# Optimization experiments

Measured on AMD Instinct MI355X. Metric: run time of the kernel, lower is better.

Reference implementation:

```python
import jax, jax.numpy as jnp
import numpy as np

NUM_EMBEDDINGS = 8192
EMBEDDING_DIM = 64
COMMITMENT_COST = 0.25


def setup_inputs() -> dict:
    key = jax.random.key(0)
    kx, ke = jax.random.split(key)
    x = jax.random.normal(kx, (32, 1024, EMBEDDING_DIM), dtype=jnp.float32)
    embeddings = jax.random.normal(ke, (NUM_EMBEDDINGS, EMBEDDING_DIM), dtype=jnp.float32)
    return {"x": x, "embeddings": embeddings}


def reference(x, embeddings):
    d = embeddings.shape[1]
    flat_x = x.reshape(-1, d)  # [N, D]
    # squared euclidean distances (argmin identical to cdist argmin):
    d2 = (
        jnp.sum(flat_x * flat_x, axis=-1, keepdims=True)
        - 2.0 * flat_x @ embeddings.T
        + jnp.sum(embeddings * embeddings, axis=-1)
    )
    encoding_indices = jnp.argmin(d2, axis=1)  # [N]
    quantized = embeddings[encoding_indices].reshape(x.shape)
    codebook_loss = jnp.mean((jax.lax.stop_gradient(quantized) - x) ** 2)
    commitment_loss = COMMITMENT_COST * jnp.mean((quantized - jax.lax.stop_gradient(x)) ** 2)
    loss = codebook_loss + commitment_loss
    # straight-through estimator
    quantized_st = x + jax.lax.stop_gradient(quantized - x)
    return quantized_st, loss, encoding_indices
```

## Files before the change

### kernel.cpp

```cpp
#include <hip/hip_runtime.h>
#include <hip/hip_bf16.h>
#include <float.h>

#define N_ROWS 32768
#define DIMS   64
#define K_EMB  8192
#define NT     (K_EMB / 16)
#define NQ     4
#define NTQ    (NT / NQ)
#define TSTAGE 4
#define NSTAGE (NTQ / TSTAGE)
#define GAP_THR 1.5e-3f

typedef __attribute__((ext_vector_type(8))) short s8v;
typedef __attribute__((ext_vector_type(4))) float f4v;
typedef __attribute__((ext_vector_type(4))) int   i4v;

#define WS_EFRAG 0
#define WS_EN2   (2 * 1024 * 1024)
#define WS_IDX   (WS_EN2 + K_EMB * 4)
#define WS_KEY   (WS_IDX + N_ROWS * 4)
#define WS_BH    (WS_KEY + N_ROWS * 8)
#define WS_SH    (WS_BH + 4 * N_ROWS * 4)
#define WS_CH    (WS_SH + 4 * N_ROWS * 4)
#define WS_CTL   (WS_CH + 4 * N_ROWS * 4)
#define WS_WL    (WS_CTL + 16)

#define OUT_LOSS (N_ROWS * DIMS)
#define OUT_IDX  (N_ROWS * DIMS + 1)

__device__ inline short bfh(float v) {
    __hip_bfloat16 h = __float2bfloat16(v);
    return __builtin_bit_cast(short, h);
}
__device__ inline float bff(short s) {
    __hip_bfloat16 h = __builtin_bit_cast(__hip_bfloat16, s);
    return __bfloat162float(h);
}

__global__ void vq_prep(const float* __restrict__ emb, short* __restrict__ efrag,
                        float* __restrict__ en2) {
    int gid = blockIdx.x * 256 + threadIdx.x;
    int t = gid >> 6, lane = gid & 63;
    int m = lane & 15, q = lane >> 4;
    const float* er = emb + (size_t)(t * 16 + m) * DIMS;
    s8v hi0, lo0, hi1, lo1;
    float ss = 0.f;
#pragma unroll
    for (int j = 0; j < 8; ++j) {
        float v0 = er[q * 8 + j];
        float v1 = er[32 + q * 8 + j];
        ss += v0 * v0 + v1 * v1;
        short h0 = bfh(v0); lo0[j] = bfh(v0 - bff(h0)); hi0[j] = h0;
        short h1 = bfh(v1); lo1[j] = bfh(v1 - bff(h1)); hi1[j] = h1;
    }
    s8v* base = (s8v*)efrag + (size_t)t * 4 * 64;
    base[0 * 64 + lane] = hi0;
    base[1 * 64 + lane] = hi1;
    base[2 * 64 + lane] = lo0;
    base[3 * 64 + lane] = lo1;
    ss += __shfl_xor(ss, 16, 64);
    ss += __shfl_xor(ss, 32, 64);
    if (q == 0) en2[t * 16 + m] = -0.5f * ss;
}

__global__ __launch_bounds__(256, 4) void vq_phase1(
    const float* __restrict__ x, const short* __restrict__ efrag,
    const float* __restrict__ en2,
    float* __restrict__ bh, float* __restrict__ sh, int* __restrict__ ch) {
    __shared__ __align__(16) char lds[2][TSTAGE * 4096];
    int tid = threadIdx.x, wid = tid >> 6, lane = tid & 63;
    int m = lane & 15, q = lane >> 4;
    int kh = blockIdx.y;
    int row0 = blockIdx.x * 128 + wid * 32;

    s8v ahi[2][2], alo[2][2];
#pragma unroll
    for (int g = 0; g < 2; ++g) {
        const float* xr = x + (size_t)(row0 + g * 16 + m) * DIMS + q * 8;
#pragma unroll
        for (int j = 0; j < 8; ++j) {
            float v0 = xr[j], v1 = xr[32 + j];
            short h0 = bfh(v0); alo[g][0][j] = bfh(v0 - bff(h0)); ahi[g][0][j] = h0;
            short h1 = bfh(v1); alo[g][1][j] = bfh(v1 - bff(h1)); ahi[g][1][j] = h1;
        }
    }

    float best[2][4], sec[2][4];
    int bc[2][4];
#pragma unroll
    for (int g = 0; g < 2; ++g)
#pragma unroll
        for (int r = 0; r < 4; ++r) { best[g][r] = -FLT_MAX; sec[g][r] = -FLT_MAX; bc[g][r] = 0; }

    const char* gsrc = (const char*)efrag + (size_t)kh * NTQ * 4096;

#pragma unroll
    for (int i = 0; i < TSTAGE; ++i)
        __builtin_amdgcn_global_load_lds(
            (const __attribute__((address_space(1))) void*)(gsrc + i * 4096 + tid * 16),
            (__attribute__((address_space(3))) void*)(&lds[0][i * 4096 + tid * 16]),
            16, 0, 0);
    __syncthreads();

    for (int s = 0; s < NSTAGE; ++s) {
        int pb = s & 1;
        if (s + 1 < NSTAGE) {
            const char* gn = gsrc + (size_t)(s + 1) * TSTAGE * 4096;
#pragma unroll
            for (int i = 0; i < TSTAGE; ++i)
                __builtin_amdgcn_global_load_lds(
                    (const __attribute__((address_space(1))) void*)(gn + i * 4096 + tid * 16),
                    (__attribute__((address_space(3))) void*)(&lds[pb ^ 1][i * 4096 + tid * 16]),
                    16, 0, 0);
        }
        const i4v* B = (const i4v*)(lds[pb]);
        int tg0 = kh * NTQ + s * TSTAGE;
        const float* ep = en2 + (size_t)tg0 * 16 + m;
#pragma unroll
        for (int tt = 0; tt < TSTAGE; ++tt) {
            i4v b0 = B[tt * 256 + 0 * 64 + lane];
            i4v b1 = B[tt * 256 + 1 * 64 + lane];
            i4v b2 = B[tt * 256 + 2 * 64 + lane];
            i4v b3 = B[tt * 256 + 3 * 64 + lane];
            float c0 = ep[tt * 16];
            int cidx = (tg0 + tt) * 16 + m;
#pragma unroll
            for (int g = 0; g < 2; ++g) {
                f4v acc = {c0, c0, c0, c0};
                acc = __builtin_amdgcn_mfma_f32_16x16x32_bf16(ahi[g][0], __builtin_bit_cast(s8v, b0), acc, 0, 0, 0);
                acc = __builtin_amdgcn_mfma_f32_16x16x32_bf16(ahi[g][1], __builtin_bit_cast(s8v, b1), acc, 0, 0, 0);
                acc = __builtin_amdgcn_mfma_f32_16x16x32_bf16(ahi[g][0], __builtin_bit_cast(s8v, b2), acc, 0, 0, 0);
                acc = __builtin_amdgcn_mfma_f32_16x16x32_bf16(ahi[g][1], __builtin_bit_cast(s8v, b3), acc, 0, 0, 0);
                acc = __builtin_amdgcn_mfma_f32_16x16x32_bf16(alo[g][0], __builtin_bit_cast(s8v, b0), acc, 0, 0, 0);
                acc = __builtin_amdgcn_mfma_f32_16x16x32_bf16(alo[g][1], __builtin_bit_cast(s8v, b1), acc, 0, 0, 0);
#pragma unroll
                for (int r = 0; r < 4; ++r) {
                    float v = acc[r];
                    bool gt = v > best[g][r];
                    sec[g][r]  = __builtin_amdgcn_fmed3f(v, sec[g][r], best[g][r]);
                    best[g][r] = fmaxf(best[g][r], v);
                    bc[g][r]   = gt ? cidx : bc[g][r];
                }
            }
        }
        __syncthreads();
    }

#pragma unroll
    for (int g = 0; g < 2; ++g)
#pragma unroll
    for (int r = 0; r < 4; ++r) {
        float b = best[g][r], s = sec[g][r];
        int c = bc[g][r];
#pragma unroll
        for (int off = 1; off < 16; off <<= 1) {
            float ob = __shfl_xor(b, off, 64);
            float os = __shfl_xor(s, off, 64);
            int   oc = __shfl_xor(c, off, 64);
            float nb = fmaxf(b, ob);
            float ns = fmaxf(fminf(b, ob), fmaxf(s, os));
            bool take = (ob > b) || (ob == b && oc < c);
            c = take ? oc : c;
            b = nb; s = ns;
        }
        if (m == 0) {
            int o = kh * N_ROWS + row0 + g * 16 + q * 4 + r;
            bh[o] = b; sh[o] = s; ch[o] = c;
        }
    }
}

__global__ void vq_merge(const float* __restrict__ bh, const float* __restrict__ sh,
                         const int* __restrict__ ch, int* __restrict__ idx_buf,
                         unsigned long long* __restrict__ key8,
                         float* __restrict__ nbv,
                         int* __restrict__ wl, int* __restrict__ wl_count) {
    int row = blockIdx.x * 256 + threadIdx.x;
    float nb = bh[row];
    int   c  = ch[row];
    float ns = -FLT_MAX;
#pragma unroll
    for (int h = 1; h < NQ; ++h) {
        float b = bh[h * N_ROWS + row];
        int   cc = ch[h * N_ROWS + row];
        if (b > nb) { ns = nb; nb = b; c = cc; }
        else        { ns = fmaxf(ns, b); }
    }
#pragma unroll
    for (int h = 0; h < NQ; ++h) ns = fmaxf(ns, sh[h * N_ROWS + row]);
    idx_buf[row] = c;
    key8[row] = 0ULL;
    nbv[row] = nb;
    if (nb - ns < GAP_THR) {
        int pos = atomicAdd(wl_count, 1);
        wl[pos] = row;
    }
}

__global__ __launch_bounds__(64) void vq_fixup(
    const float* __restrict__ x, const float* __restrict__ emb,
    const float* __restrict__ en2, const float* __restrict__ nbv,
    unsigned long long* __restrict__ key8,
    const int* __restrict__ wl, const int* __restrict__ wl_count) {
    int lane = threadIdx.x;
    int cchunk = blockIdx.x & 127;
    int rslice = blockIdx.x >> 7;
    int c = cchunk * 64 + lane;
    const float4* er = (const float4*)(emb + (size_t)c * DIMS);
    float4 e[16];
#pragma unroll
    for (int qq = 0; qq < 16; ++qq) e[qq] = er[qq];
    float c0 = en2[c];
    int cnt = *wl_count;
    for (int wi = rslice; wi < cnt; wi += 16) {
        int row = wl[wi];
        const float4* xr = (const float4*)(x + (size_t)row * DIMS);
        float d = 0.f;
#pragma unroll
        for (int qq = 0; qq < 16; ++qq) {
            float4 ee = e[qq];
            float4 xx = xr[qq];
            d += ee.x * xx.x + ee.y * xx.y + ee.z * xx.z + ee.w * xx.w;
        }
        float bf_ = d + c0;
        int bc_ = c;
#pragma unroll
        for (int off = 1; off < 64; off <<= 1) {
            float of = __shfl_xor(bf_, off, 64);
            int   oc = __shfl_xor(bc_, off, 64);
            if (of > bf_ || (of == bf_ && oc < bc_)) { bf_ = of; bc_ = oc; }
        }
        if (lane == 0 && bf_ >= nbv[row] - GAP_THR) {
            unsigned int u = __float_as_uint(bf_);
            unsigned int sb = ((int)u < 0) ? ~u : (u | 0x80000000u);
            unsigned long long key = ((unsigned long long)sb << 32) | (unsigned int)(~bc_);
            atomicMax(&key8[row], key);
        }
    }
}

__global__ void vq_gather(const float* __restrict__ x, const float* __restrict__ emb,
                          const int* __restrict__ idx_buf,
                          const unsigned long long* __restrict__ key8,
                          float* __restrict__ out, double* __restrict__ loss_acc) {
    int row = blockIdx.x * blockDim.x + threadIdx.x;
    unsigned long long k = key8[row];
    int idx = k ? (int)(~(unsigned int)k) : idx_buf[row];
    const float4* ev = (const float4*)(emb + (size_t)idx * DIMS);
    const float4* xv = (const float4*)(x + (size_t)row * DIMS);
    float4* ov = (float4*)(out + (size_t)row * DIMS);
    float s = 0.f;
#pragma unroll
    for (int qq = 0; qq < 16; ++qq) {
        float4 ee = ev[qq];
        float4 xx = xv[qq];
        float dx = ee.x - xx.x, dy = ee.y - xx.y, dz = ee.z - xx.z, dw = ee.w - xx.w;
        s += dx * dx + dy * dy + dz * dz + dw * dw;
        ov[qq] = ee;
    }
#pragma unroll
    for (int off = 32; off > 0; off >>= 1) s += __shfl_down(s, off, 64);
    if ((threadIdx.x & 63) == 0) atomicAdd(loss_acc, (double)s);
    out[OUT_IDX + row] = (float)idx;
}

__global__ void vq_loss(const double* __restrict__ acc, float* __restrict__ out) {
    out[OUT_LOSS] = (float)(1.25 * (*acc) / (double)(N_ROWS * DIMS));
}

extern "C" void kernel_launch(void* const* d_in, const int* in_sizes, int n_in,
                              void* d_out, int out_size, void* d_ws, size_t ws_size,
                              hipStream_t stream) {
    const float* x   = (const float*)d_in[0];
    const float* emb = (const float*)d_in[1];
    float* out = (float*)d_out;
    char*  ws  = (char*)d_ws;

    short* efrag   = (short*)(ws + WS_EFRAG);
    float* en2     = (float*)(ws + WS_EN2);
    int*   idx_buf = (int*)(ws + WS_IDX);
    unsigned long long* key8 = (unsigned long long*)(ws + WS_KEY);
    float* bhb     = (float*)(ws + WS_BH);
    float* shb     = (float*)(ws + WS_SH);
    int*   chb     = (int*)(ws + WS_CH);
    double* loss_acc = (double*)(ws + WS_CTL);
    int*   wl_count  = (int*)(ws + WS_CTL + 8);
    int*   wl        = (int*)(ws + WS_WL);

    hipMemsetAsync(ws + WS_CTL, 0, 16, stream);

    vq_prep<<<(NT * 64) / 256, 256, 0, stream>>>(emb, efrag, en2);
    vq_phase1<<<dim3(N_ROWS / 128, NQ), 256, 0, stream>>>(x, efrag, en2, bhb, shb, chb);
    vq_merge<<<N_ROWS / 256, 256, 0, stream>>>(bhb, shb, chb, idx_buf, key8, bhb, wl, wl_count);
    vq_fixup<<<2048, 64, 0, stream>>>(x, emb, en2, bhb, key8, wl, wl_count);
    vq_gather<<<N_ROWS / 256, 256, 0, stream>>>(x, emb, idx_buf, key8, out, loss_acc);
    vq_loss<<<1, 1, 0, stream>>>(loss_acc, out);
}
```

Baseline: 193.8 us.

## Widen per-wave row blocking and split codebook sixteen ways in distance kernel

Each wave now handles 64 rows (four 16-row groups) instead of 32, so every codebook fragment read from LDS feeds twice as many MFMA chains. The codebook is split into 16 slices instead of 4 so the grid keeps enough blocks, and the launch bound drops to 3 waves per SIMD to make room for the larger register state. The separate memset of the control words is folded into the prep kernel to save one launch. The cost is four times more partial best/second-best records for the merge kernel to read, shorter per-block pipelines, and lower occupancy.

```diff
diff --git a/kernel.cpp b/kernel.cpp
--- a/kernel.cpp
+++ b/kernel.cpp
@@ -6,10 +6,11 @@
 #define DIMS   64
 #define K_EMB  8192
 #define NT     (K_EMB / 16)
-#define NQ     4
+#define NQ     16
 #define NTQ    (NT / NQ)
 #define TSTAGE 4
 #define NSTAGE (NTQ / TSTAGE)
+#define RG     4
 #define GAP_THR 1.5e-3f
 
 typedef __attribute__((ext_vector_type(8))) short s8v;
@@ -21,9 +22,9 @@
 #define WS_IDX   (WS_EN2 + K_EMB * 4)
 #define WS_KEY   (WS_IDX + N_ROWS * 4)
 #define WS_BH    (WS_KEY + N_ROWS * 8)
-#define WS_SH    (WS_BH + 4 * N_ROWS * 4)
-#define WS_CH    (WS_SH + 4 * N_ROWS * 4)
-#define WS_CTL   (WS_CH + 4 * N_ROWS * 4)
+#define WS_SH    (WS_BH + NQ * N_ROWS * 4)
+#define WS_CH    (WS_SH + NQ * N_ROWS * 4)
+#define WS_CTL   (WS_CH + NQ * N_ROWS * 4)
 #define WS_WL    (WS_CTL + 16)
 
 #define OUT_LOSS (N_ROWS * DIMS)
@@ -39,7 +40,8 @@
 }
 
 __global__ void vq_prep(const float* __restrict__ emb, short* __restrict__ efrag,
-                        float* __restrict__ en2) {
+                        float* __restrict__ en2, int4* __restrict__ ctl) {
+    if (blockIdx.x == 0 && threadIdx.x == 0) *ctl = make_int4(0, 0, 0, 0);
     int gid = blockIdx.x * 256 + threadIdx.x;
     int t = gid >> 6, lane = gid & 63;
     int m = lane & 15, q = lane >> 4;
@@ -64,7 +66,7 @@
     if (q == 0) en2[t * 16 + m] = -0.5f * ss;
 }
 
-__global__ __launch_bounds__(256, 4) void vq_phase1(
+__global__ __launch_bounds__(256, 3) void vq_phase1(
     const float* __restrict__ x, const short* __restrict__ efrag,
     const float* __restrict__ en2,
     float* __restrict__ bh, float* __restrict__ sh, int* __restrict__ ch) {
@@ -72,11 +74,11 @@
     int tid = threadIdx.x, wid = tid >> 6, lane = tid & 63;
     int m = lane & 15, q = lane >> 4;
     int kh = blockIdx.y;
-    int row0 = blockIdx.x * 128 + wid * 32;
-
-    s8v ahi[2][2], alo[2][2];
-#pragma unroll
-    for (int g = 0; g < 2; ++g) {
+    int row0 = blockIdx.x * 256 + wid * 64;
+
+    s8v ahi[RG][2], alo[RG][2];
+#pragma unroll
+    for (int g = 0; g < RG; ++g) {
         const float* xr = x + (size_t)(row0 + g * 16 + m) * DIMS + q * 8;
 #pragma unroll
         for (int j = 0; j < 8; ++j) {
@@ -86,10 +88,10 @@
         }
     }
 
-    float best[2][4], sec[2][4];
-    int bc[2][4];
-#pragma unroll
-    for (int g = 0; g < 2; ++g)
+    float best[RG][4], sec[RG][4];
+    int bc[RG][4];
+#pragma unroll
+    for (int g = 0; g < RG; ++g)
 #pragma unroll
         for (int r = 0; r < 4; ++r) { best[g][r] = -FLT_MAX; sec[g][r] = -FLT_MAX; bc[g][r] = 0; }
 
@@ -125,10 +127,11 @@
             i4v b3 = B[tt * 256 + 3 * 64 + lane];
             float c0 = ep[tt * 16];
             int cidx = (tg0 + tt) * 16 + m;
-#pragma unroll
-            for (int g = 0; g < 2; ++g) {
-                f4v acc = {c0, c0, c0, c0};
-                acc = __builtin_amdgcn_mfma_f32_16x16x32_bf16(ahi[g][0], __builtin_bit_cast(s8v, b0), acc, 0, 0, 0);
+            f4v cinit = {c0, c0, c0, c0};
+#pragma unroll
+            for (int g = 0; g < RG; ++g) {
+                f4v acc;
+                acc = __builtin_amdgcn_mfma_f32_16x16x32_bf16(ahi[g][0], __builtin_bit_cast(s8v, b0), cinit, 0, 0, 0);
                 acc = __builtin_amdgcn_mfma_f32_16x16x32_bf16(ahi[g][1], __builtin_bit_cast(s8v, b1), acc, 0, 0, 0);
                 acc = __builtin_amdgcn_mfma_f32_16x16x32_bf16(ahi[g][0], __builtin_bit_cast(s8v, b2), acc, 0, 0, 0);
                 acc = __builtin_amdgcn_mfma_f32_16x16x32_bf16(ahi[g][1], __builtin_bit_cast(s8v, b3), acc, 0, 0, 0);
@@ -148,7 +151,7 @@
     }
 
 #pragma unroll
-    for (int g = 0; g < 2; ++g)
+    for (int g = 0; g < RG; ++g)
 #pragma unroll
     for (int r = 0; r < 4; ++r) {
         float b = best[g][r], s = sec[g][r];
@@ -288,10 +291,8 @@
     int*   wl_count  = (int*)(ws + WS_CTL + 8);
     int*   wl        = (int*)(ws + WS_WL);
 
-    hipMemsetAsync(ws + WS_CTL, 0, 16, stream);
-
-    vq_prep<<<(NT * 64) / 256, 256, 0, stream>>>(emb, efrag, en2);
-    vq_phase1<<<dim3(N_ROWS / 128, NQ), 256, 0, stream>>>(x, efrag, en2, bhb, shb, chb);
+    vq_prep<<<(NT * 64) / 256, 256, 0, stream>>>(emb, efrag, en2, (int4*)(ws + WS_CTL));
+    vq_phase1<<<dim3(N_ROWS / 256, NQ), 256, 0, stream>>>(x, efrag, en2, bhb, shb, chb);
     vq_merge<<<N_ROWS / 256, 256, 0, stream>>>(bhb, shb, chb, idx_buf, key8, bhb, wl, wl_count);
     vq_fixup<<<2048, 64, 0, stream>>>(x, emb, en2, bhb, key8, wl, wl_count);
     vq_gather<<<N_ROWS / 256, 256, 0, stream>>>(x, emb, idx_buf, key8, out, loss_acc);
```

Measured after the change: 202.5 us. 4.5% more time.
